# Performance work log

Measured on AMD Instinct MI355X. Metric: run time of the kernel, lower is better.

The kernel has to match this reference:

```python
import jax, jax.numpy as jnp
import numpy as np

N = 50000          # nodes per node type
F = 256            # input feature dim
C = 256            # hidden_channels
H, D = 8, 32       # heads, head_dim (C = H*D)
E = 200000         # edges per edge type
OUT = 16           # out_channels
SRC = (0, 1, 0)    # edge type -> source node-type index (user,item)
DST = (1, 0, 0)    # edge type -> destination node-type index
LABELED = 1        # labeled_class = 'item'


def setup_inputs() -> dict:
    key = jax.random.key(0)
    ks = jax.random.split(key, 24)
    s = 0.06  # ~1/sqrt(256) init scale
    inp = {
        'x': jax.random.normal(ks[0], (2, N, F), jnp.float32),
        'edge_index': jax.random.randint(ks[1], (3, 2, E), 0, N, jnp.int64),
        'lin_w': jax.random.normal(ks[2], (2, F, C), jnp.float32) * s,
        'lin_b': jnp.zeros((2, C), jnp.float32),
        'k_w': jax.random.normal(ks[3], (2, C, C), jnp.float32) * s,
        'k_b': jnp.zeros((2, C), jnp.float32),
        'q_w': jax.random.normal(ks[4], (2, C, C), jnp.float32) * s,
        'q_b': jnp.zeros((2, C), jnp.float32),
        'v_w': jax.random.normal(ks[5], (2, C, C), jnp.float32) * s,
        'v_b': jnp.zeros((2, C), jnp.float32),
        'a_w': jax.random.normal(ks[6], (2, C, C), jnp.float32) * s,
        'a_b': jnp.zeros((2, C), jnp.float32),
        'skip': jnp.ones((2,), jnp.float32),
        'a_rel': jax.random.normal(ks[7], (3, H, D, D), jnp.float32) * (1.0 / np.sqrt(D)),
        'm_rel': jax.random.normal(ks[8], (3, H, D, D), jnp.float32) * (1.0 / np.sqrt(D)),
        'p_rel': jnp.ones((3, H), jnp.float32),
        'out_w': jax.random.normal(ks[9], (C, OUT), jnp.float32) * s,
        'out_b': jnp.zeros((OUT,), jnp.float32),
    }
    return inp


def _segment_softmax(alpha, idx, n):
    # alpha: [E, H], idx: [E] destination node ids
    amax = jax.ops.segment_max(alpha, idx, num_segments=n)
    amax = jnp.where(jnp.isfinite(amax), amax, 0.0)
    ex = jnp.exp(alpha - amax[idx])
    den = jax.ops.segment_sum(ex, idx, num_segments=n)
    return ex / (den[idx] + 1e-16)


def reference(x, edge_index, lin_w, lin_b, k_w, k_b, q_w, q_b, v_w, v_b,
              a_w, a_b, skip, a_rel, m_rel, p_rel, out_w, out_b):
    # per-node-type input Linear + ReLU
    h = jax.nn.relu(jnp.einsum('tnf,tfc->tnc', x, lin_w) + lin_b[:, None, :])

    def proj(w, b):
        return (jnp.einsum('tnc,tce->tne', h, w) + b[:, None, :]).reshape(2, N, H, D)

    k = proj(k_w, k_b)
    q = proj(q_w, q_b)
    v = proj(v_w, v_b)

    agg = jnp.zeros((2, N, H, D), h.dtype)
    for t in range(3):  # fixed small loop over edge types
        s, d = SRC[t], DST[t]
        src_idx, dst_idx = edge_index[t, 0], edge_index[t, 1]
        # relation-specific transforms of source keys / values
        k_rel = jnp.einsum('nhd,hde->nhe', k[s], a_rel[t])
        v_rel = jnp.einsum('nhd,hde->nhe', v[s], m_rel[t])
        # per-edge attention logits [E, H]
        alpha = (q[d][dst_idx] * k_rel[src_idx]).sum(-1) * p_rel[t] / (D ** 0.5)
        alpha = _segment_softmax(alpha, dst_idx, N)
        msg = v_rel[src_idx] * alpha[..., None]          # [E, H, D]
        agg = agg.at[d].add(jax.ops.segment_sum(msg, dst_idx, num_segments=N))

    o = agg.reshape(2, N, C)
    o = jnp.einsum('tnc,tce->tne', jax.nn.gelu(o, approximate=False), a_w) + a_b[:, None, :]
    beta = jax.nn.sigmoid(skip)[:, None, None]
    o = beta * o + (1.0 - beta) * h                      # skip connection (in == out dims)

    return o[LABELED] @ out_w + out_b                    # logits for labeled_class='item'
```

## Files before the change

kernel.cpp:

```cpp
#include <hip/hip_runtime.h>
#include <hip/hip_bf16.h>

using u16 = unsigned short;
using u32 = unsigned int;

#define NNODES 50000
#define NEDGE  200000
#define DEGCAP 64
#define NT     3125

__device__ __forceinline__ float blo2f(u32 u) { u32 v = u << 16; float f; __builtin_memcpy(&f, &v, 4); return f; }
__device__ __forceinline__ float bhi2f(u32 u) { u32 v = u & 0xffff0000u; float f; __builtin_memcpy(&f, &v, 4); return f; }
__device__ __forceinline__ float b2f(u16 u) { u32 v = ((u32)u) << 16; float f; __builtin_memcpy(&f, &v, 4); return f; }
__device__ __forceinline__ u16 f2b(float f) {
  __hip_bfloat16 h = __float2bfloat16(f);
  u16 r; __builtin_memcpy(&r, &h, 2); return r;
}
__device__ __forceinline__ float gelu_exact(float x) {
  return 0.5f * x * (1.f + erff(x * 0.70710678118654752f));
}

__device__ __forceinline__ void gload16(const void* gp, void* lp) {
  __builtin_amdgcn_global_load_lds(
      (__attribute__((address_space(1))) u32*)(const_cast<void*>(gp)),
      (__attribute__((address_space(3))) u32*)lp, 16, 0, 0);
}

__device__ __forceinline__ void wait_vm0() {
  asm volatile("s_waitcnt vmcnt(0)" ::: "memory");
}

typedef __bf16 bh8 __attribute__((ext_vector_type(8)));
typedef float f32x4 __attribute__((ext_vector_type(4)));

struct GArg { const u16* A; const u16* B; const float* bias; u16* C; };

__device__ __forceinline__ void stage_tile(const u16* At, u16* buf, int lane) {
#pragma unroll
  for (int i = 0; i < 8; ++i) {
    const int row = i * 2 + (lane >> 5);
    const int c   = (lane & 31) ^ (row & 7);
    gload16(At + (size_t)row * 256 + c * 8, buf + i * 512 + lane * 8);
  }
}

template <int MODE>
__launch_bounds__(256, 3)
__global__ void gemm_v7(GArg g0, GArg g1, GArg g2,
                        const u16* __restrict__ hbl, const float* __restrict__ skipv)
{
  GArg ga = (blockIdx.z == 0) ? g0 : ((blockIdx.z == 1) ? g1 : g2);
  const int tid = threadIdx.x;
  const int lane = tid & 63;
  const int wave = tid >> 6;
  const int lr = lane & 15;
  const int lq = lane >> 4;
  const int colbase = blockIdx.y * 32;

  __shared__ alignas(16) u16 lds[4][4096];
  __shared__ alignas(16) u16 pat[4][640];
  u16* buf = &lds[wave][0];
  u16* wl  = &pat[wave][0];

  bh8 B0[8], B1[8];
  {
    const u16* bp0 = ga.B + (size_t)(colbase + lr) * 256 + lq * 8;
    const u16* bp1 = bp0 + 16 * 256;
#pragma unroll
    for (int ks = 0; ks < 8; ++ks) {
      B0[ks] = *(const bh8*)(bp0 + ks * 32);
      B1[ks] = *(const bh8*)(bp1 + ks * 32);
    }
  }
  const float bias0 = ga.bias[colbase + lr];
  const float bias1 = ga.bias[colbase + 16 + lr];
  float beta = 0.f, omb = 0.f;
  if (MODE == 2) { beta = 1.f / (1.f + __expf(-skipv[0])); omb = 1.f - beta; }

  int foff[8];
#pragma unroll
  for (int ks = 0; ks < 8; ++ks)
    foff[ks] = lr * 256 + (((ks * 4 + lq) ^ (lr & 7)) * 8);

  const int wt0 = blockIdx.x * 4 + wave;
  const int wts = gridDim.x * 4;

  for (int t = wt0; t < NT; t += wts) {
    stage_tile(ga.A + (size_t)t * 4096, buf, lane);
    wait_vm0();

    bh8 ab[8];
#pragma unroll
    for (int ks = 0; ks < 8; ++ks) ab[ks] = *(const bh8*)(buf + foff[ks]);

    f32x4 acc0 = {0.f, 0.f, 0.f, 0.f};
    f32x4 acc1 = {0.f, 0.f, 0.f, 0.f};
#pragma unroll
    for (int ks = 0; ks < 8; ++ks) {
      acc0 = __builtin_amdgcn_mfma_f32_16x16x32_bf16(ab[ks], B0[ks], acc0, 0, 0, 0);
      acc1 = __builtin_amdgcn_mfma_f32_16x16x32_bf16(ab[ks], B1[ks], acc1, 0, 0, 0);
    }

#pragma unroll
    for (int r = 0; r < 4; ++r) {
      float v0 = acc0[r] + bias0;
      float v1 = acc1[r] + bias1;
      if (MODE == 0) { v0 = fmaxf(v0, 0.f); v1 = fmaxf(v1, 0.f); }
      wl[(lq * 4 + r) * 40 + lr]      = f2b(v0);
      wl[(lq * 4 + r) * 40 + 16 + lr] = f2b(v1);
    }
    const int rrow = lane >> 2, rseg = lane & 3;
    const uint4 pv = *(const uint4*)(wl + rrow * 40 + rseg * 8);
    const size_t cb = ((size_t)t * 16 + rrow) * 256 + colbase + rseg * 8;
    if (MODE == 2) {
      const uint4 hv = *(const uint4*)(hbl + cb);
      const u32 p[4] = {pv.x, pv.y, pv.z, pv.w};
      const u32 h[4] = {hv.x, hv.y, hv.z, hv.w};
      u32 o[4];
#pragma unroll
      for (int j = 0; j < 4; ++j) {
        const float a0 = blo2f(p[j]), a1 = bhi2f(p[j]);
        const float h0 = blo2f(h[j]), h1 = bhi2f(h[j]);
        o[j] = (u32)f2b(beta * a0 + omb * h0) | ((u32)f2b(beta * a1 + omb * h1) << 16);
      }
      uint4 ov; ov.x = o[0]; ov.y = o[1]; ov.z = o[2]; ov.w = o[3];
      *(uint4*)(ga.C + cb) = ov;
    } else {
      *(uint4*)(ga.C + cb) = pv;
    }
  }
}

__global__ void cvt_x_k(const float* __restrict__ x, u16* __restrict__ xb) {
  const int id = blockIdx.x * 256 + threadIdx.x;
  if (id >= (2 * NNODES * 256) / 8) return;
  const float4 a = ((const float4*)x)[id * 2];
  const float4 b = ((const float4*)x)[id * 2 + 1];
  uint4 o;
  o.x = (u32)f2b(a.x) | ((u32)f2b(a.y) << 16);
  o.y = (u32)f2b(a.z) | ((u32)f2b(a.w) << 16);
  o.z = (u32)f2b(b.x) | ((u32)f2b(b.y) << 16);
  o.w = (u32)f2b(b.z) | ((u32)f2b(b.w) << 16);
  ((uint4*)xb)[id] = o;
}

__global__ void prep_w_k(const float* __restrict__ lin_w, const float* __restrict__ q_w,
                         const float* __restrict__ a_w, const float* __restrict__ k_w,
                         const float* __restrict__ v_w, const float* __restrict__ k_b,
                         const float* __restrict__ v_b, const float* __restrict__ a_rel,
                         const float* __restrict__ m_rel, const float* __restrict__ out_w,
                         u16* __restrict__ lin0T, u16* __restrict__ lin1T,
                         u16* __restrict__ qT, u16* __restrict__ aT,
                         u16* __restrict__ kfT, u16* __restrict__ vfT,
                         u16* __restrict__ owT,
                         float* __restrict__ bkf, float* __restrict__ bvf)
{
  const int tid = blockIdx.x * 256 + threadIdx.x;
  const int nn = tid >> 8, kk = tid & 255;
  switch (blockIdx.y) {
    case 0: lin0T[tid] = f2b(lin_w[kk * 256 + nn]); break;
    case 1: lin1T[tid] = f2b(lin_w[65536 + kk * 256 + nn]); break;
    case 2: qT[tid] = f2b(q_w[65536 + kk * 256 + nn]); break;
    case 3: aT[tid] = f2b(a_w[65536 + kk * 256 + nn]); break;
    case 4: {
      const int h = nn >> 5, e = nn & 31;
      float s = 0.f;
      for (int d = 0; d < 32; ++d) s += k_w[kk * 256 + h * 32 + d] * a_rel[(h * 32 + d) * 32 + e];
      kfT[tid] = f2b(s);
      if (kk == 0) {
        float sb = 0.f;
        for (int d = 0; d < 32; ++d) sb += k_b[h * 32 + d] * a_rel[(h * 32 + d) * 32 + e];
        bkf[nn] = sb;
      }
      break;
    }
    case 5: {
      const int h = nn >> 5, e = nn & 31;
      float s = 0.f;
      for (int d = 0; d < 32; ++d) s += v_w[kk * 256 + h * 32 + d] * m_rel[(h * 32 + d) * 32 + e];
      vfT[tid] = f2b(s);
      if (kk == 0) {
        float sb = 0.f;
        for (int d = 0; d < 32; ++d) sb += v_b[h * 32 + d] * m_rel[(h * 32 + d) * 32 + e];
        bvf[nn] = sb;
      }
      break;
    }
    default:
      if (tid < 4096) owT[tid] = f2b(out_w[kk * 16 + nn]);
      break;
  }
}

__global__ void scatter_k(const int* __restrict__ ei, int* __restrict__ cnt, int* __restrict__ srcl) {
  const int e = blockIdx.x * 256 + threadIdx.x;
  if (e >= NEDGE) return;
  const int src = ei[e];
  const int dst = ei[NEDGE + e];
  if ((unsigned)dst >= NNODES || (unsigned)src >= NNODES) return;
  const int pos = atomicAdd(&cnt[dst], 1);
  if (pos < DEGCAP) srcl[(size_t)dst * DEGCAP + pos] = src;
}

__global__ void edge_agg_k(const u16* __restrict__ qb, const u16* __restrict__ krel,
                           const u16* __restrict__ vrel, const int* __restrict__ cnt,
                           const int* __restrict__ srcl, const float* __restrict__ prel,
                           u16* __restrict__ g)
{
  const int node = (blockIdx.x * blockDim.x + threadIdx.x) >> 6;
  if (node >= NNODES) return;
  const int lane = threadIdx.x & 63;
  const int hh = lane >> 3;
  const int off = hh * 32 + (lane & 7) * 4;
  const float scale = prel[hh] * 0.17677669529663687f;
  const uint2 qv = *(const uint2*)(qb + (size_t)node * 256 + off);
  const float q0 = blo2f(qv.x) * scale, q1 = bhi2f(qv.x) * scale;
  const float q2 = blo2f(qv.y) * scale, q3 = bhi2f(qv.y) * scale;
  int dg = cnt[node]; if (dg > DEGCAP) dg = DEGCAP;
  const int* sl = srcl + (size_t)node * DEGCAP;
  float den = 0.f, a0 = 0.f, a1 = 0.f, a2 = 0.f, a3 = 0.f;
  for (int i = 0; i < dg; ++i) {
    const int src = sl[i];
    const uint2 kv = *(const uint2*)(krel + (size_t)src * 256 + off);
    float p = q0 * blo2f(kv.x) + q1 * bhi2f(kv.x) + q2 * blo2f(kv.y) + q3 * bhi2f(kv.y);
    p += __shfl_xor(p, 1);
    p += __shfl_xor(p, 2);
    p += __shfl_xor(p, 4);
    const float ex = __expf(p);
    const uint2 vv = *(const uint2*)(vrel + (size_t)src * 256 + off);
    den += ex;
    a0 += ex * blo2f(vv.x); a1 += ex * bhi2f(vv.x);
    a2 += ex * blo2f(vv.y); a3 += ex * bhi2f(vv.y);
  }
  float r0 = 0.f, r1 = 0.f, r2 = 0.f, r3 = 0.f;
  if (dg > 0) {
    const float inv = 1.f / den;
    r0 = gelu_exact(a0 * inv); r1 = gelu_exact(a1 * inv);
    r2 = gelu_exact(a2 * inv); r3 = gelu_exact(a3 * inv);
  }
  uint2 gv;
  gv.x = (u32)f2b(r0) | ((u32)f2b(r1) << 16);
  gv.y = (u32)f2b(r2) | ((u32)f2b(r3) << 16);
  *(uint2*)(g + (size_t)node * 256 + off) = gv;
}

__launch_bounds__(256, 3)
__global__ void out_v7(const u16* __restrict__ o, const u16* __restrict__ owT,
                       const float* __restrict__ ob, float* __restrict__ out)
{
  const int tid = threadIdx.x;
  const int lane = tid & 63;
  const int wave = tid >> 6;
  const int lr = lane & 15;
  const int lq = lane >> 4;

  __shared__ alignas(16) u16 lds[4][4096];
  u16* buf = &lds[wave][0];

  bh8 bw[8];
  {
    const u16* bp = owT + (size_t)lr * 256 + lq * 8;
#pragma unroll
    for (int ks = 0; ks < 8; ++ks) bw[ks] = *(const bh8*)(bp + ks * 32);
  }
  const float bv = ob[lr];

  int foff[8];
#pragma unroll
  for (int ks = 0; ks < 8; ++ks)
    foff[ks] = lr * 256 + (((ks * 4 + lq) ^ (lr & 7)) * 8);

  const int wt0 = blockIdx.x * 4 + wave;
  const int wts = gridDim.x * 4;

  for (int t = wt0; t < NT; t += wts) {
    stage_tile(o + (size_t)t * 4096, buf, lane);
    wait_vm0();
    f32x4 acc = {0.f, 0.f, 0.f, 0.f};
#pragma unroll
    for (int ks = 0; ks < 8; ++ks)
      acc = __builtin_amdgcn_mfma_f32_16x16x32_bf16(*(const bh8*)(buf + foff[ks]), bw[ks], acc, 0, 0, 0);
#pragma unroll
    for (int r = 0; r < 4; ++r)
      out[((size_t)t * 16 + lq * 4 + r) * 16 + lr] = acc[r] + bv;
  }
}

extern "C" void kernel_launch(void* const* d_in, const int* in_sizes, int n_in,
                              void* d_out, int out_size, void* d_ws, size_t ws_size,
                              hipStream_t stream)
{
  const float* x     = (const float*)d_in[0];
  const int*   ei    = (const int*)d_in[1];
  const float* lin_w = (const float*)d_in[2];
  const float* lin_b = (const float*)d_in[3];
  const float* k_w   = (const float*)d_in[4];
  const float* k_b   = (const float*)d_in[5];
  const float* q_w   = (const float*)d_in[6];
  const float* q_b   = (const float*)d_in[7];
  const float* v_w   = (const float*)d_in[8];
  const float* v_b   = (const float*)d_in[9];
  const float* a_w   = (const float*)d_in[10];
  const float* a_b   = (const float*)d_in[11];
  const float* skipv = (const float*)d_in[12];
  const float* a_rel = (const float*)d_in[13];
  const float* m_rel = (const float*)d_in[14];
  const float* p_rel = (const float*)d_in[15];
  const float* out_w = (const float*)d_in[16];
  const float* out_b = (const float*)d_in[17];
  char* ws = (char*)d_ws;

  u16*  xb    = (u16*)(ws + 0);
  u16*  h0    = (u16*)(ws + 51200000);
  u16*  h1    = (u16*)(ws + 76800000);
  u16*  qb    = (u16*)(ws + 102400000);
  u16*  gbuf  = (u16*)(ws + 128000000);
  u16*  krel  = (u16*)(ws + 0);
  u16*  vrel  = (u16*)(ws + 25600000);
  u16*  obuf  = (u16*)(ws + 0);
  char* W     = ws + 153600000;
  u16*  lin0T = (u16*)(W + 0);
  u16*  lin1T = (u16*)(W + 131072);
  u16*  qT    = (u16*)(W + 2 * 131072);
  u16*  aT    = (u16*)(W + 3 * 131072);
  u16*  kfT   = (u16*)(W + 4 * 131072);
  u16*  vfT   = (u16*)(W + 5 * 131072);
  u16*  owT   = (u16*)(W + 6 * 131072);
  float* bkf  = (float*)(W + 6 * 131072 + 8192);
  float* bvf  = (float*)(W + 6 * 131072 + 9216);
  int*  cnt   = (int*)(W + 6 * 131072 + 10240);
  int*  srcl  = (int*)(W + 6 * 131072 + 10240 + 200000);

  hipMemsetAsync(cnt, 0, NNODES * sizeof(int), stream);
  prep_w_k<<<dim3(256, 7), 256, 0, stream>>>(lin_w, q_w, a_w, k_w, v_w, k_b, v_b,
                                             a_rel, m_rel, out_w,
                                             lin0T, lin1T, qT, aT, kfT, vfT, owT, bkf, bvf);
  scatter_k<<<(NEDGE + 255) / 256, 256, 0, stream>>>(ei, cnt, srcl);
  cvt_x_k<<<12500, 256, 0, stream>>>(x, xb);

  {
    GArg a0{xb, lin0T, lin_b, h0};
    GArg a1{xb + (size_t)NNODES * 256, lin1T, lin_b + 256, h1};
    gemm_v7<0><<<dim3(48, 8, 2), 256, 0, stream>>>(a0, a1, a0, nullptr, nullptr);
  }
  {
    GArg a0{h1, qT, q_b + 256, qb};
    GArg a1{h0, kfT, bkf, krel};
    GArg a2{h0, vfT, bvf, vrel};
    gemm_v7<1><<<dim3(32, 8, 3), 256, 0, stream>>>(a0, a1, a2, nullptr, nullptr);
  }
  edge_agg_k<<<12500, 256, 0, stream>>>(qb, krel, vrel, cnt, srcl, p_rel, gbuf);
  {
    GArg a0{gbuf, aT, a_b + 256, obuf};
    gemm_v7<2><<<dim3(96, 8, 1), 256, 0, stream>>>(a0, a0, a0, h1, skipv + 1);
  }
  out_v7<<<192, 256, 0, stream>>>(obuf, owT, out_b, (float*)d_out);
}
```

Measured before the change: 363.2 us.

## Fold a_w into out_w and share A tiles across columns in GEMM

The a_w projection, skip blend and output projection are folded algebraically into one 512x16 weight and bias, precomputed in the prep kernel. The final stage becomes a single K=512 GEMM over [gelu-agg | h1], removing the 256x256 GEMM over all item nodes and its intermediate buffer. The main GEMM is restructured so one block loads each 16-row A tile once and each wave covers 64 output columns, with double-buffered LDS staging. Folding a_w and out_w in bf16 changes rounding, and holding more B registers per wave lowers occupancy.

```diff
diff --git a/kernel.cpp b/kernel.cpp
--- a/kernel.cpp
+++ b/kernel.cpp
@@ -29,6 +29,9 @@
 __device__ __forceinline__ void wait_vm0() {
   asm volatile("s_waitcnt vmcnt(0)" ::: "memory");
 }
+__device__ __forceinline__ void wait_vm2() {
+  asm volatile("s_waitcnt vmcnt(2)" ::: "memory");
+}
 
 typedef __bf16 bh8 __attribute__((ext_vector_type(8)));
 typedef float f32x4 __attribute__((ext_vector_type(4)));
@@ -44,90 +47,93 @@
   }
 }
 
+__device__ __forceinline__ void stage_tile_blk(const u16* At, u16* buf, int wave, int lane) {
+#pragma unroll
+  for (int i = 0; i < 2; ++i) {
+    const int row = wave * 4 + i * 2 + (lane >> 5);
+    const int c   = (lane & 31) ^ (row & 7);
+    gload16(At + (size_t)row * 256 + c * 8, buf + wave * 1024 + i * 512 + lane * 8);
+  }
+}
+
 template <int MODE>
-__launch_bounds__(256, 3)
-__global__ void gemm_v7(GArg g0, GArg g1, GArg g2,
-                        const u16* __restrict__ hbl, const float* __restrict__ skipv)
+__launch_bounds__(256, 2)
+__global__ void gemm_v8(GArg g0, GArg g1, GArg g2)
 {
   GArg ga = (blockIdx.z == 0) ? g0 : ((blockIdx.z == 1) ? g1 : g2);
-  const int tid = threadIdx.x;
+  const int tid  = threadIdx.x;
   const int lane = tid & 63;
   const int wave = tid >> 6;
   const int lr = lane & 15;
   const int lq = lane >> 4;
-  const int colbase = blockIdx.y * 32;
-
-  __shared__ alignas(16) u16 lds[4][4096];
-  __shared__ alignas(16) u16 pat[4][640];
-  u16* buf = &lds[wave][0];
-  u16* wl  = &pat[wave][0];
-
-  bh8 B0[8], B1[8];
-  {
-    const u16* bp0 = ga.B + (size_t)(colbase + lr) * 256 + lq * 8;
-    const u16* bp1 = bp0 + 16 * 256;
-#pragma unroll
-    for (int ks = 0; ks < 8; ++ks) {
-      B0[ks] = *(const bh8*)(bp0 + ks * 32);
-      B1[ks] = *(const bh8*)(bp1 + ks * 32);
-    }
-  }
-  const float bias0 = ga.bias[colbase + lr];
-  const float bias1 = ga.bias[colbase + 16 + lr];
-  float beta = 0.f, omb = 0.f;
-  if (MODE == 2) { beta = 1.f / (1.f + __expf(-skipv[0])); omb = 1.f - beta; }
+  const int colbase = wave * 64;
+
+  __shared__ alignas(16) u16 lds[2][4096];
+  __shared__ alignas(16) u16 pat[4][1152];
+  u16* wl = &pat[wave][0];
+
+  bh8 B[4][8];
+#pragma unroll
+  for (int s = 0; s < 4; ++s) {
+    const u16* bp = ga.B + (size_t)(colbase + s * 16 + lr) * 256 + lq * 8;
+#pragma unroll
+    for (int ks = 0; ks < 8; ++ks) B[s][ks] = *(const bh8*)(bp + ks * 32);
+  }
+  float bias[4];
+#pragma unroll
+  for (int s = 0; s < 4; ++s) bias[s] = ga.bias[colbase + s * 16 + lr];
 
   int foff[8];
 #pragma unroll
   for (int ks = 0; ks < 8; ++ks)
     foff[ks] = lr * 256 + (((ks * 4 + lq) ^ (lr & 7)) * 8);
 
-  const int wt0 = blockIdx.x * 4 + wave;
-  const int wts = gridDim.x * 4;
-
-  for (int t = wt0; t < NT; t += wts) {
-    stage_tile(ga.A + (size_t)t * 4096, buf, lane);
-    wait_vm0();
-
+  const int t0 = blockIdx.x;
+  const int ts = gridDim.x;
+
+  stage_tile_blk(ga.A + (size_t)t0 * 4096, &lds[0][0], wave, lane);
+  int cur = 0;
+
+  for (int t = t0; t < NT; t += ts) {
+    const int tn = t + ts;
+    if (tn < NT)
+      stage_tile_blk(ga.A + (size_t)tn * 4096, &lds[cur ^ 1][0], wave, lane);
+    wait_vm2();
+    __builtin_amdgcn_s_barrier();
+
+    const u16* buf = &lds[cur][0];
     bh8 ab[8];
 #pragma unroll
     for (int ks = 0; ks < 8; ++ks) ab[ks] = *(const bh8*)(buf + foff[ks]);
 
-    f32x4 acc0 = {0.f, 0.f, 0.f, 0.f};
-    f32x4 acc1 = {0.f, 0.f, 0.f, 0.f};
+    f32x4 acc[4];
+#pragma unroll
+    for (int s = 0; s < 4; ++s) acc[s] = (f32x4){0.f, 0.f, 0.f, 0.f};
 #pragma unroll
     for (int ks = 0; ks < 8; ++ks) {
-      acc0 = __builtin_amdgcn_mfma_f32_16x16x32_bf16(ab[ks], B0[ks], acc0, 0, 0, 0);
-      acc1 = __builtin_amdgcn_mfma_f32_16x16x32_bf16(ab[ks], B1[ks], acc1, 0, 0, 0);
-    }
-
-#pragma unroll
-    for (int r = 0; r < 4; ++r) {
-      float v0 = acc0[r] + bias0;
-      float v1 = acc1[r] + bias1;
-      if (MODE == 0) { v0 = fmaxf(v0, 0.f); v1 = fmaxf(v1, 0.f); }
-      wl[(lq * 4 + r) * 40 + lr]      = f2b(v0);
-      wl[(lq * 4 + r) * 40 + 16 + lr] = f2b(v1);
-    }
-    const int rrow = lane >> 2, rseg = lane & 3;
-    const uint4 pv = *(const uint4*)(wl + rrow * 40 + rseg * 8);
-    const size_t cb = ((size_t)t * 16 + rrow) * 256 + colbase + rseg * 8;
-    if (MODE == 2) {
-      const uint4 hv = *(const uint4*)(hbl + cb);
-      const u32 p[4] = {pv.x, pv.y, pv.z, pv.w};
-      const u32 h[4] = {hv.x, hv.y, hv.z, hv.w};
-      u32 o[4];
-#pragma unroll
-      for (int j = 0; j < 4; ++j) {
-        const float a0 = blo2f(p[j]), a1 = bhi2f(p[j]);
-        const float h0 = blo2f(h[j]), h1 = bhi2f(h[j]);
-        o[j] = (u32)f2b(beta * a0 + omb * h0) | ((u32)f2b(beta * a1 + omb * h1) << 16);
-      }
-      uint4 ov; ov.x = o[0]; ov.y = o[1]; ov.z = o[2]; ov.w = o[3];
-      *(uint4*)(ga.C + cb) = ov;
-    } else {
-      *(uint4*)(ga.C + cb) = pv;
-    }
+#pragma unroll
+      for (int s = 0; s < 4; ++s)
+        acc[s] = __builtin_amdgcn_mfma_f32_16x16x32_bf16(ab[ks], B[s][ks], acc[s], 0, 0, 0);
+    }
+
+#pragma unroll
+    for (int s = 0; s < 4; ++s) {
+#pragma unroll
+      for (int r = 0; r < 4; ++r) {
+        float v = acc[s][r] + bias[s];
+        if (MODE == 0) v = fmaxf(v, 0.f);
+        wl[(lq * 4 + r) * 72 + s * 16 + lr] = f2b(v);
+      }
+    }
+#pragma unroll
+    for (int j = 0; j < 2; ++j) {
+      const int row = (lane >> 3) + j * 8;
+      const int seg = lane & 7;
+      const uint4 pv = *(const uint4*)(wl + row * 72 + seg * 8);
+      *(uint4*)(ga.C + ((size_t)t * 16 + row) * 256 + colbase + seg * 8) = pv;
+    }
+    __builtin_amdgcn_s_barrier();
+    cur ^= 1;
   }
 }
 
@@ -149,10 +155,12 @@
                          const float* __restrict__ v_w, const float* __restrict__ k_b,
                          const float* __restrict__ v_b, const float* __restrict__ a_rel,
                          const float* __restrict__ m_rel, const float* __restrict__ out_w,
+                         const float* __restrict__ a_b, const float* __restrict__ out_b,
+                         const float* __restrict__ skipv,
                          u16* __restrict__ lin0T, u16* __restrict__ lin1T,
-                         u16* __restrict__ qT, u16* __restrict__ aT,
+                         u16* __restrict__ qT,
                          u16* __restrict__ kfT, u16* __restrict__ vfT,
-                         u16* __restrict__ owT,
+                         u16* __restrict__ WcT, float* __restrict__ bfin,
                          float* __restrict__ bkf, float* __restrict__ bvf)
 {
   const int tid = blockIdx.x * 256 + threadIdx.x;
@@ -161,8 +169,7 @@
     case 0: lin0T[tid] = f2b(lin_w[kk * 256 + nn]); break;
     case 1: lin1T[tid] = f2b(lin_w[65536 + kk * 256 + nn]); break;
     case 2: qT[tid] = f2b(q_w[65536 + kk * 256 + nn]); break;
-    case 3: aT[tid] = f2b(a_w[65536 + kk * 256 + nn]); break;
-    case 4: {
+    case 3: {
       const int h = nn >> 5, e = nn & 31;
       float s = 0.f;
       for (int d = 0; d < 32; ++d) s += k_w[kk * 256 + h * 32 + d] * a_rel[(h * 32 + d) * 32 + e];
@@ -174,7 +181,7 @@
       }
       break;
     }
-    case 5: {
+    case 4: {
       const int h = nn >> 5, e = nn & 31;
       float s = 0.f;
       for (int d = 0; d < 32; ++d) s += v_w[kk * 256 + h * 32 + d] * m_rel[(h * 32 + d) * 32 + e];
@@ -186,9 +193,29 @@
       }
       break;
     }
-    default:
-      if (tid < 4096) owT[tid] = f2b(out_w[kk * 16 + nn]);
+    default: {
+      const float beta = 1.f / (1.f + __expf(-skipv[1]));
+      if (tid < 8192) {
+        const int j = tid & 15;
+        const int k = tid >> 4;
+        float s;
+        if (k < 256) {
+          float acc = 0.f;
+          for (int d = 0; d < 256; ++d)
+            acc += a_w[65536 + k * 256 + d] * out_w[d * 16 + j];
+          s = beta * acc;
+        } else {
+          s = (1.f - beta) * out_w[(k - 256) * 16 + j];
+        }
+        WcT[j * 512 + k] = f2b(s);
+      }
+      if (tid < 16) {
+        float acc = 0.f;
+        for (int c = 0; c < 256; ++c) acc += a_b[256 + c] * out_w[c * 16 + tid];
+        bfin[tid] = beta * acc + out_b[tid];
+      }
       break;
+    }
   }
 }
 
@@ -244,9 +271,10 @@
   *(uint2*)(g + (size_t)node * 256 + off) = gv;
 }
 
-__launch_bounds__(256, 3)
-__global__ void out_v7(const u16* __restrict__ o, const u16* __restrict__ owT,
-                       const float* __restrict__ ob, float* __restrict__ out)
+__launch_bounds__(256, 2)
+__global__ void final_k(const u16* __restrict__ g, const u16* __restrict__ h1,
+                        const u16* __restrict__ WcT, const float* __restrict__ bfin,
+                        float* __restrict__ out)
 {
   const int tid = threadIdx.x;
   const int lane = tid & 63;
@@ -254,16 +282,16 @@
   const int lr = lane & 15;
   const int lq = lane >> 4;
 
-  __shared__ alignas(16) u16 lds[4][4096];
+  __shared__ alignas(16) u16 lds[4][8192];
   u16* buf = &lds[wave][0];
 
-  bh8 bw[8];
+  bh8 B[16];
   {
-    const u16* bp = owT + (size_t)lr * 256 + lq * 8;
-#pragma unroll
-    for (int ks = 0; ks < 8; ++ks) bw[ks] = *(const bh8*)(bp + ks * 32);
-  }
-  const float bv = ob[lr];
+    const u16* bp = WcT + (size_t)lr * 512 + lq * 8;
+#pragma unroll
+    for (int ks = 0; ks < 16; ++ks) B[ks] = *(const bh8*)(bp + ks * 32);
+  }
+  const float bv = bfin[lr];
 
   int foff[8];
 #pragma unroll
@@ -274,12 +302,16 @@
   const int wts = gridDim.x * 4;
 
   for (int t = wt0; t < NT; t += wts) {
-    stage_tile(o + (size_t)t * 4096, buf, lane);
+    stage_tile(g  + (size_t)t * 4096, buf,        lane);
+    stage_tile(h1 + (size_t)t * 4096, buf + 4096, lane);
     wait_vm0();
     f32x4 acc = {0.f, 0.f, 0.f, 0.f};
 #pragma unroll
     for (int ks = 0; ks < 8; ++ks)
-      acc = __builtin_amdgcn_mfma_f32_16x16x32_bf16(*(const bh8*)(buf + foff[ks]), bw[ks], acc, 0, 0, 0);
+      acc = __builtin_amdgcn_mfma_f32_16x16x32_bf16(*(const bh8*)(buf + foff[ks]), B[ks], acc, 0, 0, 0);
+#pragma unroll
+    for (int ks = 0; ks < 8; ++ks)
+      acc = __builtin_amdgcn_mfma_f32_16x16x32_bf16(*(const bh8*)(buf + 4096 + foff[ks]), B[ks + 8], acc, 0, 0, 0);
 #pragma unroll
     for (int r = 0; r < 4; ++r)
       out[((size_t)t * 16 + lq * 4 + r) * 16 + lr] = acc[r] + bv;
@@ -317,42 +349,37 @@
   u16*  gbuf  = (u16*)(ws + 128000000);
   u16*  krel  = (u16*)(ws + 0);
   u16*  vrel  = (u16*)(ws + 25600000);
-  u16*  obuf  = (u16*)(ws + 0);
   char* W     = ws + 153600000;
   u16*  lin0T = (u16*)(W + 0);
   u16*  lin1T = (u16*)(W + 131072);
   u16*  qT    = (u16*)(W + 2 * 131072);
-  u16*  aT    = (u16*)(W + 3 * 131072);
-  u16*  kfT   = (u16*)(W + 4 * 131072);
-  u16*  vfT   = (u16*)(W + 5 * 131072);
-  u16*  owT   = (u16*)(W + 6 * 131072);
-  float* bkf  = (float*)(W + 6 * 131072 + 8192);
-  float* bvf  = (float*)(W + 6 * 131072 + 9216);
-  int*  cnt   = (int*)(W + 6 * 131072 + 10240);
-  int*  srcl  = (int*)(W + 6 * 131072 + 10240 + 200000);
+  u16*  kfT   = (u16*)(W + 3 * 131072);
+  u16*  vfT   = (u16*)(W + 4 * 131072);
+  u16*  WcT   = (u16*)(W + 5 * 131072);
+  float* bfin = (float*)(W + 5 * 131072 + 16384);
+  float* bkf  = (float*)(W + 5 * 131072 + 17408);
+  float* bvf  = (float*)(W + 5 * 131072 + 18432);
+  int*  cnt   = (int*)(W + 5 * 131072 + 19456);
+  int*  srcl  = (int*)(W + 5 * 131072 + 19456 + 200000);
 
   hipMemsetAsync(cnt, 0, NNODES * sizeof(int), stream);
-  prep_w_k<<<dim3(256, 7), 256, 0, stream>>>(lin_w, q_w, a_w, k_w, v_w, k_b, v_b,
-                                             a_rel, m_rel, out_w,
-                                             lin0T, lin1T, qT, aT, kfT, vfT, owT, bkf, bvf);
+  prep_w_k<<<dim3(256, 6), 256, 0, stream>>>(lin_w, q_w, a_w, k_w, v_w, k_b, v_b,
+                                             a_rel, m_rel, out_w, a_b, out_b, skipv,
+                                             lin0T, lin1T, qT, kfT, vfT, WcT, bfin, bkf, bvf);
   scatter_k<<<(NEDGE + 255) / 256, 256, 0, stream>>>(ei, cnt, srcl);
   cvt_x_k<<<12500, 256, 0, stream>>>(x, xb);
 
   {
     GArg a0{xb, lin0T, lin_b, h0};
     GArg a1{xb + (size_t)NNODES * 256, lin1T, lin_b + 256, h1};
-    gemm_v7<0><<<dim3(48, 8, 2), 256, 0, stream>>>(a0, a1, a0, nullptr, nullptr);
+    gemm_v8<0><<<dim3(256, 1, 2), 256, 0, stream>>>(a0, a1, a0);
   }
   {
     GArg a0{h1, qT, q_b + 256, qb};
     GArg a1{h0, kfT, bkf, krel};
     GArg a2{h0, vfT, bvf, vrel};
-    gemm_v7<1><<<dim3(32, 8, 3), 256, 0, stream>>>(a0, a1, a2, nullptr, nullptr);
+    gemm_v8<1><<<dim3(170, 1, 3), 256, 0, stream>>>(a0, a1, a2);
   }
   edge_agg_k<<<12500, 256, 0, stream>>>(qb, krel, vrel, cnt, srcl, p_rel, gbuf);
-  {
-    GArg a0{gbuf, aT, a_b + 256, obuf};
-    gemm_v7<2><<<dim3(96, 8, 1), 256, 0, stream>>>(a0, a0, a0, h1, skipv + 1);
-  }
-  out_v7<<<192, 256, 0, stream>>>(obuf, owT, out_b, (float*)d_out);
-}
+  final_k<<<512, 256, 0, stream>>>(gbuf, h1, WcT, bfin, (float*)d_out);
+}
```

After: 346.6 us. -4.6%, faster.
